# Kernel tuning notes

Hardware: AMD Instinct MI355X
Metric: run time of the kernel (lower is better)

The kernel has to match this reference:

```python
import jax, jax.numpy as jnp
import numpy as np

# FP4 (E2M1) code table: nibble = [sign(1) | exp(2) | mantissa(1)]
# magnitudes for codes 0..7: 0, 0.5, 1, 1.5, 2, 3, 4, 6; codes 8..15 are negated.
_MAG = np.array([0.0, 0.5, 1.0, 1.5, 2.0, 3.0, 4.0, 6.0], dtype=np.float32)
FP4_LUT = jnp.asarray(np.concatenate([_MAG, -_MAG]))  # [16]

BLOCK = 16  # scale-factor block size along in_features


def setup_inputs() -> dict:
    key = jax.random.key(0)
    k0, k1, k2, k3, k4 = jax.random.split(key, 5)
    M, K, N = 32, 8192, 8192  # tokens, in_features, out_features
    inp = jax.random.normal(k0, (M, K), dtype=jnp.float32)
    qweight = jax.random.randint(k1, (N, K // 2), 0, 256, dtype=jnp.int32)  # packed FP4 pairs
    scales = jax.random.uniform(k2, (N, K // BLOCK), dtype=jnp.float32)      # per-block scales
    amax = jax.random.uniform(k3, (1,), dtype=jnp.float32) + 0.5             # global scale
    bias = jax.random.normal(k4, (N,), dtype=jnp.float32)
    return {"input": inp, "qweight": qweight, "scales": scales, "amax": amax, "bias": bias}


def _dequantize(qweight, scales, amax):
    N = qweight.shape[0]
    low = qweight & 0xF            # first element of each pair
    high = (qweight >> 4) & 0xF    # second element
    nibbles = jnp.stack([low, high], axis=-1).reshape(N, -1)  # [N, K]
    vals = FP4_LUT[nibbles]                                   # [N, K] fp4 values
    # per-block scaling: block of BLOCK contiguous in-features shares one scale
    w = (vals.reshape(N, -1, BLOCK) * scales[..., None]).reshape(N, -1)
    return w * amax[0]


def reference(input, qweight, scales, amax, bias):
    weight = _dequantize(qweight, scales, amax)   # [N, K] full-precision weight
    return input @ weight.T + bias                # F.linear
```

## Files before the change

### kernel.cpp

```cpp
#include <hip/hip_runtime.h>
#include <hip/hip_bf16.h>

#define M_DIM 32
#define K_DIM 8192
#define N_DIM 8192
#define KS 8
#define KCH (K_DIM / KS)
#define CHK 128
#define NCHK (KCH / CHK)
#define STEPS (CHK / 32)
#define NPB 64
#define MAIN_BLOCKS ((N_DIM / NPB) * KS)

#define QW_ROWI4 (K_DIM / 8)
#define SC_ROW (K_DIM / 16)

#define QROW 17
#define AROW 136
#define SROW 9

typedef _Float16 half8   __attribute__((ext_vector_type(8)));
typedef _Float16 half4_t __attribute__((ext_vector_type(4)));
typedef float    floatx4 __attribute__((ext_vector_type(4)));
typedef float    floatx2 __attribute__((ext_vector_type(2)));

__device__ __forceinline__ uint32_t dec2(uint32_t b) {
  uint32_t c0 = b & 0xFu, c1 = (b >> 4) & 0xFu;
  uint32_t m0 = c0 & 7u, m1 = c1 & 7u;
  uint32_t t0 = min(28u * m0, m0 + 28u);
  uint32_t t1 = min(28u * m1, m1 + 28u);
  return (t0 << 9) | ((c0 & 8u) << 12)
       | (t1 << 25) | ((c1 & 8u) << 28);
}

__device__ __forceinline__ half8 decode8p(uint32_t q, _Float16 s) {
  union { uint32_t u[4]; half8 h; } w;
  w.u[0] = dec2(q & 0xFFu);
  w.u[1] = dec2((q >> 8) & 0xFFu);
  w.u[2] = dec2((q >> 16) & 0xFFu);
  w.u[3] = dec2((q >> 24) & 0xFFu);
  half8 sv = {s, s, s, s, s, s, s, s};
  return w.h * sv;
}

__global__ void prep_kernel(const floatx4* __restrict__ in4,
                            half4_t* __restrict__ a16,
                            const floatx4* __restrict__ bias4,
                            floatx4* __restrict__ out4) {
  int b = blockIdx.x;
  if (b < (M_DIM * N_DIM / 4 / 256)) {
    int idx = b * 256 + threadIdx.x;
    out4[idx] = bias4[idx & (N_DIM / 4 - 1)];
  } else {
    int idx = (b - (M_DIM * N_DIM / 4 / 256)) * 256 + threadIdx.x;
    floatx4 f = in4[idx];
    half4_t h;
    h[0] = (_Float16)f[0]; h[1] = (_Float16)f[1];
    h[2] = (_Float16)f[2]; h[3] = (_Float16)f[3];
    a16[idx] = h;
  }
}

template <bool F16A>
__global__ __launch_bounds__(256, 4) void fp4_linear_kernel(
    const void*  __restrict__ Av,
    const int4*  __restrict__ qw4,
    const float* __restrict__ scales,
    const float* __restrict__ amaxp,
    float*       __restrict__ out)
{
  __shared__ uint32_t Qs[NPB * QROW];
  __shared__ _Float16 As[M_DIM * AROW];
  __shared__ float    Ss[NPB * SROW];

  const int t    = threadIdx.x;
  const int lane = t & 63;
  const int w    = t >> 6;
  const int ks   = blockIdx.x & (KS - 1);
  const int nb   = blockIdx.x >> 3;
  const int n0   = nb * NPB;
  const int kb   = ks * KCH;
  const float amax = amaxp[0];

  const int qr = t >> 4, qc = t & 15;
  const int4* qsrc = qw4 + (size_t)(n0 + qr) * QW_ROWI4 + ks * (KCH / 8) + qc;
  const int sr = t >> 2, sh = t & 3;
  const float* ssrc = scales + (size_t)(n0 + sr) * SC_ROW + ks * (KCH / 16) + sh * 2;
  const int ar16 = t >> 4, ac16 = t & 15;
  const _Float16* asrc16 =
      (const _Float16*)Av + (size_t)ar16 * K_DIM + kb + ac16 * 8;
  const int ar32 = t >> 5, ac32 = t & 31;
  const float* asrc32 = (const float*)Av + (size_t)ar32 * K_DIM + kb + ac32 * 4;

  int4    qreg[4];
  half8   areg16[2];
  floatx4 areg32[4];
  floatx2 sreg;

  {
#pragma unroll
    for (int j = 0; j < 4; ++j)
      qreg[j] = qsrc[(size_t)j * 16 * QW_ROWI4];
    if (F16A) {
#pragma unroll
      for (int j = 0; j < 2; ++j)
        areg16[j] = *(const half8*)(asrc16 + (size_t)j * 16 * K_DIM);
    } else {
#pragma unroll
      for (int j = 0; j < 4; ++j)
        areg32[j] = *(const floatx4*)(asrc32 + (size_t)j * 8 * K_DIM);
    }
    sreg = *(const floatx2*)ssrc;
  }

  const int row  = lane & 15;
  const int quad = lane >> 4;
  const int nloc = w * 16;
  const uint32_t* qAp = &Qs[(nloc + row) * QROW];
  const _Float16* a0p = &As[row * AROW];
  const _Float16* a1p = &As[(row + 16) * AROW];
  const float*    sAp = &Ss[(nloc + row) * SROW];

  floatx4 acc0 = {0.f, 0.f, 0.f, 0.f};
  floatx4 acc1 = {0.f, 0.f, 0.f, 0.f};

  for (int c = 0; c < NCHK; ++c) {
    if (c) __syncthreads();

#pragma unroll
    for (int j = 0; j < 4; ++j) {
      uint32_t pk = ((uint32_t)qreg[j].x & 0xFFu)
                  | (((uint32_t)qreg[j].y & 0xFFu) << 8)
                  | (((uint32_t)qreg[j].z & 0xFFu) << 16)
                  | (((uint32_t)qreg[j].w & 0xFFu) << 24);
      Qs[(j * 16 + qr) * QROW + qc] = pk;
    }
    if (F16A) {
#pragma unroll
      for (int j = 0; j < 2; ++j)
        *(half8*)&As[(j * 16 + ar16) * AROW + ac16 * 8] = areg16[j];
    } else {
#pragma unroll
      for (int j = 0; j < 4; ++j) {
        floatx4 f = areg32[j];
        half4_t h;
        h[0] = (_Float16)f[0]; h[1] = (_Float16)f[1];
        h[2] = (_Float16)f[2]; h[3] = (_Float16)f[3];
        *(half4_t*)&As[(j * 8 + ar32) * AROW + ac32 * 4] = h;
      }
    }
    {
      float* sd = &Ss[sr * SROW + sh * 2];
      sd[0] = sreg[0] * amax; sd[1] = sreg[1] * amax;
    }
    __syncthreads();

    if (c + 1 < NCHK) {
      const int co = c + 1;
#pragma unroll
      for (int j = 0; j < 4; ++j)
        qreg[j] = qsrc[(size_t)j * 16 * QW_ROWI4 + co * (CHK / 8)];
      if (F16A) {
#pragma unroll
        for (int j = 0; j < 2; ++j)
          areg16[j] = *(const half8*)(asrc16 + (size_t)j * 16 * K_DIM + co * CHK);
      } else {
#pragma unroll
        for (int j = 0; j < 4; ++j)
          areg32[j] = *(const floatx4*)(asrc32 + (size_t)j * 8 * K_DIM + co * CHK);
      }
      sreg = *(const floatx2*)(ssrc + co * (CHK / 16));
    }

#pragma unroll
    for (int it = 0; it < STEPS; ++it) {
      const uint32_t qA = qAp[it * 4 + quad];
      const _Float16 sA = (_Float16)sAp[it * 2 + (quad >> 1)];
      half8 bA = decode8p(qA, sA);
      half8 a0 = *(const half8*)(a0p + it * 32 + quad * 8);
      half8 a1 = *(const half8*)(a1p + it * 32 + quad * 8);
      acc0 = __builtin_amdgcn_mfma_f32_16x16x32_f16(a0, bA, acc0, 0, 0, 0);
      acc1 = __builtin_amdgcn_mfma_f32_16x16x32_f16(a1, bA, acc1, 0, 0, 0);
    }
  }

#pragma unroll
  for (int r = 0; r < 4; ++r) {
    const int m = quad * 4 + r;
    atomicAdd(&out[(size_t)m * N_DIM + n0 + nloc + row], acc0[r]);
    atomicAdd(&out[(size_t)(m + 16) * N_DIM + n0 + nloc + row], acc1[r]);
  }
}

extern "C" void kernel_launch(void* const* d_in, const int* in_sizes, int n_in,
                              void* d_out, int out_size, void* d_ws, size_t ws_size,
                              hipStream_t stream) {
  const float* inp    = (const float*)d_in[0];
  const int4*  qw4    = (const int4*)d_in[1];
  const float* scales = (const float*)d_in[2];
  const float* amaxp  = (const float*)d_in[3];
  const float* bias   = (const float*)d_in[4];
  float* out = (float*)d_out;

  const size_t a16_bytes = (size_t)M_DIM * K_DIM * sizeof(_Float16);
  const int init_blocks = M_DIM * N_DIM / 4 / 256;
  const int conv_blocks = M_DIM * K_DIM / 4 / 256;

  if (ws_size >= a16_bytes) {
    _Float16* Af16 = (_Float16*)d_ws;
    prep_kernel<<<init_blocks + conv_blocks, 256, 0, stream>>>(
        (const floatx4*)inp, (half4_t*)Af16, (const floatx4*)bias,
        (floatx4*)out);
    fp4_linear_kernel<true><<<MAIN_BLOCKS, 256, 0, stream>>>(
        Af16, qw4, scales, amaxp, out);
  } else {
    prep_kernel<<<init_blocks, 256, 0, stream>>>(
        nullptr, nullptr, (const floatx4*)bias, (floatx4*)out);
    fp4_linear_kernel<false><<<MAIN_BLOCKS, 256, 0, stream>>>(
        inp, qw4, scales, amaxp, out);
  }
}
```

Measured before the change: 214.9 us.

## Double-buffer global prefetch registers to issue loads two chunks ahead

Replaces the single register prefetch set with two alternating sets (A/B), so global loads for chunk c+1 are issued before the LDS store and barrier of chunk c rather than after. This deepens the load pipeline to hide global memory latency of the qweight stream. It costs extra VGPRs, which may reduce occupancy under launch_bounds(256,4).

Result: no change. 214.2 us (-0.3%).

```diff
diff --git a/kernel.cpp b/kernel.cpp
--- a/kernel.cpp
+++ b/kernel.cpp
@@ -92,25 +92,73 @@
   const int ar32 = t >> 5, ac32 = t & 31;
   const float* asrc32 = (const float*)Av + (size_t)ar32 * K_DIM + kb + ac32 * 4;
 
-  int4    qreg[4];
-  half8   areg16[2];
-  floatx4 areg32[4];
-  floatx2 sreg;
-
-  {
-#pragma unroll
-    for (int j = 0; j < 4; ++j)
-      qreg[j] = qsrc[(size_t)j * 16 * QW_ROWI4];
-    if (F16A) {
-#pragma unroll
-      for (int j = 0; j < 2; ++j)
-        areg16[j] = *(const half8*)(asrc16 + (size_t)j * 16 * K_DIM);
-    } else {
-#pragma unroll
-      for (int j = 0; j < 4; ++j)
-        areg32[j] = *(const floatx4*)(asrc32 + (size_t)j * 8 * K_DIM);
-    }
-    sreg = *(const floatx2*)ssrc;
+  int4    qregA[4], qregB[4];
+  half8   aregA16[2], aregB16[2];
+  floatx4 aregA32[4], aregB32[4];
+  floatx2 sregA, sregB;
+
+#define ISSUE_A(CO)                                                         \
+  if ((CO) < NCHK) {                                                        \
+    _Pragma("unroll")                                                       \
+    for (int j = 0; j < 4; ++j)                                             \
+      qregA[j] = qsrc[(size_t)j * 16 * QW_ROWI4 + (CO) * (CHK / 8)];        \
+    if (F16A) {                                                             \
+      _Pragma("unroll")                                                     \
+      for (int j = 0; j < 2; ++j)                                           \
+        aregA16[j] = *(const half8*)(asrc16 + (size_t)j * 16 * K_DIM + (CO) * CHK); \
+    } else {                                                                \
+      _Pragma("unroll")                                                     \
+      for (int j = 0; j < 4; ++j)                                           \
+        aregA32[j] = *(const floatx4*)(asrc32 + (size_t)j * 8 * K_DIM + (CO) * CHK); \
+    }                                                                       \
+    sregA = *(const floatx2*)(ssrc + (CO) * (CHK / 16));                    \
+  }
+
+#define ISSUE_B(CO)                                                         \
+  if ((CO) < NCHK) {                                                        \
+    _Pragma("unroll")                                                       \
+    for (int j = 0; j < 4; ++j)                                             \
+      qregB[j] = qsrc[(size_t)j * 16 * QW_ROWI4 + (CO) * (CHK / 8)];        \
+    if (F16A) {                                                             \
+      _Pragma("unroll")                                                     \
+      for (int j = 0; j < 2; ++j)                                           \
+        aregB16[j] = *(const half8*)(asrc16 + (size_t)j * 16 * K_DIM + (CO) * CHK); \
+    } else {                                                                \
+      _Pragma("unroll")                                                     \
+      for (int j = 0; j < 4; ++j)                                           \
+        aregB32[j] = *(const floatx4*)(asrc32 + (size_t)j * 8 * K_DIM + (CO) * CHK); \
+    }                                                                       \
+    sregB = *(const floatx2*)(ssrc + (CO) * (CHK / 16));                    \
+  }
+
+#define STORE_LDS(QR, AR16, AR32, SR)                                       \
+  {                                                                         \
+    _Pragma("unroll")                                                       \
+    for (int j = 0; j < 4; ++j) {                                           \
+      uint32_t pk = ((uint32_t)QR[j].x & 0xFFu)                             \
+                  | (((uint32_t)QR[j].y & 0xFFu) << 8)                      \
+                  | (((uint32_t)QR[j].z & 0xFFu) << 16)                     \
+                  | (((uint32_t)QR[j].w & 0xFFu) << 24);                    \
+      Qs[(j * 16 + qr) * QROW + qc] = pk;                                   \
+    }                                                                       \
+    if (F16A) {                                                             \
+      _Pragma("unroll")                                                     \
+      for (int j = 0; j < 2; ++j)                                           \
+        *(half8*)&As[(j * 16 + ar16) * AROW + ac16 * 8] = AR16[j];          \
+    } else {                                                                \
+      _Pragma("unroll")                                                     \
+      for (int j = 0; j < 4; ++j) {                                         \
+        floatx4 f = AR32[j];                                                \
+        half4_t h;                                                          \
+        h[0] = (_Float16)f[0]; h[1] = (_Float16)f[1];                       \
+        h[2] = (_Float16)f[2]; h[3] = (_Float16)f[3];                       \
+        *(half4_t*)&As[(j * 8 + ar32) * AROW + ac32 * 4] = h;               \
+      }                                                                     \
+    }                                                                       \
+    {                                                                       \
+      float* sd = &Ss[sr * SROW + sh * 2];                                  \
+      sd[0] = SR[0] * amax; sd[1] = SR[1] * amax;                           \
+    }                                                                       \
   }
 
   const int row  = lane & 15;
@@ -124,65 +172,41 @@
   floatx4 acc0 = {0.f, 0.f, 0.f, 0.f};
   floatx4 acc1 = {0.f, 0.f, 0.f, 0.f};
 
-  for (int c = 0; c < NCHK; ++c) {
-    if (c) __syncthreads();
+#define COMPUTE_CHUNK                                                       \
+  {                                                                         \
+    _Pragma("unroll")                                                       \
+    for (int it = 0; it < STEPS; ++it) {                                    \
+      const uint32_t qA = qAp[it * 4 + quad];                               \
+      const _Float16 sA = (_Float16)sAp[it * 2 + (quad >> 1)];              \
+      half8 bA = decode8p(qA, sA);                                          \
+      half8 a0 = *(const half8*)(a0p + it * 32 + quad * 8);                 \
+      half8 a1 = *(const half8*)(a1p + it * 32 + quad * 8);                 \
+      acc0 = __builtin_amdgcn_mfma_f32_16x16x32_f16(a0, bA, acc0, 0, 0, 0); \
+      acc1 = __builtin_amdgcn_mfma_f32_16x16x32_f16(a1, bA, acc1, 0, 0, 0); \
+    }                                                                       \
+  }
+
+  ISSUE_A(0);
 
 #pragma unroll
-    for (int j = 0; j < 4; ++j) {
-      uint32_t pk = ((uint32_t)qreg[j].x & 0xFFu)
-                  | (((uint32_t)qreg[j].y & 0xFFu) << 8)
-                  | (((uint32_t)qreg[j].z & 0xFFu) << 16)
-                  | (((uint32_t)qreg[j].w & 0xFFu) << 24);
-      Qs[(j * 16 + qr) * QROW + qc] = pk;
-    }
-    if (F16A) {
-#pragma unroll
-      for (int j = 0; j < 2; ++j)
-        *(half8*)&As[(j * 16 + ar16) * AROW + ac16 * 8] = areg16[j];
-    } else {
-#pragma unroll
-      for (int j = 0; j < 4; ++j) {
-        floatx4 f = areg32[j];
-        half4_t h;
-        h[0] = (_Float16)f[0]; h[1] = (_Float16)f[1];
-        h[2] = (_Float16)f[2]; h[3] = (_Float16)f[3];
-        *(half4_t*)&As[(j * 8 + ar32) * AROW + ac32 * 4] = h;
-      }
-    }
-    {
-      float* sd = &Ss[sr * SROW + sh * 2];
-      sd[0] = sreg[0] * amax; sd[1] = sreg[1] * amax;
-    }
+  for (int cc = 0; cc < NCHK / 2; ++cc) {
+    const int e = 2 * cc;
+    ISSUE_B(e + 1);
+    if (e) __syncthreads();
+    STORE_LDS(qregA, aregA16, aregA32, sregA);
     __syncthreads();
-
-    if (c + 1 < NCHK) {
-      const int co = c + 1;
-#pragma unroll
-      for (int j = 0; j < 4; ++j)
-        qreg[j] = qsrc[(size_t)j * 16 * QW_ROWI4 + co * (CHK / 8)];
-      if (F16A) {
-#pragma unroll
-        for (int j = 0; j < 2; ++j)
-          areg16[j] = *(const half8*)(asrc16 + (size_t)j * 16 * K_DIM + co * CHK);
-      } else {
-#pragma unroll
-        for (int j = 0; j < 4; ++j)
-          areg32[j] = *(const floatx4*)(asrc32 + (size_t)j * 8 * K_DIM + co * CHK);
-      }
-      sreg = *(const floatx2*)(ssrc + co * (CHK / 16));
-    }
-
-#pragma unroll
-    for (int it = 0; it < STEPS; ++it) {
-      const uint32_t qA = qAp[it * 4 + quad];
-      const _Float16 sA = (_Float16)sAp[it * 2 + (quad >> 1)];
-      half8 bA = decode8p(qA, sA);
-      half8 a0 = *(const half8*)(a0p + it * 32 + quad * 8);
-      half8 a1 = *(const half8*)(a1p + it * 32 + quad * 8);
-      acc0 = __builtin_amdgcn_mfma_f32_16x16x32_f16(a0, bA, acc0, 0, 0, 0);
-      acc1 = __builtin_amdgcn_mfma_f32_16x16x32_f16(a1, bA, acc1, 0, 0, 0);
-    }
-  }
+    COMPUTE_CHUNK;
+    ISSUE_A(e + 2);
+    __syncthreads();
+    STORE_LDS(qregB, aregB16, aregB32, sregB);
+    __syncthreads();
+    COMPUTE_CHUNK;
+  }
+
+#undef ISSUE_A
+#undef ISSUE_B
+#undef STORE_LDS
+#undef COMPUTE_CHUNK
 
 #pragma unroll
   for (int r = 0; r < 4; ++r) {
```
